# Kernel optimization log

Measured on AMD Instinct MI355X. Metric: run time of the kernel, lower is better.

The kernel has to match this reference:

```python
import jax, jax.numpy as jnp
import numpy as np

B, H, W, C = 512, 7, 7, 768


def _conv3(v, k, b):
    # 1-channel conv1d, kernel size 3, padding 1. v: (B, L), k: (3,), b: scalar
    vp = jnp.pad(v, ((0, 0), (1, 1)))
    return k[0] * vp[:, :-2] + k[1] * vp[:, 1:-1] + k[2] * vp[:, 2:] + b


def setup_inputs() -> dict:
    key = jax.random.key(0)
    ks = jax.random.split(key, 32)
    n = lambda i, shape, s=0.02: jax.random.normal(ks[i], shape, dtype=jnp.float32) * s
    inp = {
        "x": jax.random.normal(ks[0], (B, H, W, C), dtype=jnp.float32),
        # 1x1 Conv2d(dim,dim) weights stored as (out,in)
        "Wh": n(1, (C, C)), "bh": n(2, (C,)),
        "Ww": n(3, (C, C)), "bw": n(4, (C,)),
        "Ws": n(5, (C, C)), "bs": n(6, (C,)),
        # Conv1d(1,1,1) -> scalar weight/bias
        "convH_w": n(7, ()), "convH_b": n(8, ()),
        "convH2_k": n(9, (3,)), "convH2_b": n(10, ()),
        # Conv1d(2,1,1)
        "mixhw_k": n(11, (2,)), "mixhw_b": n(12, ()),
        "mixhw2_k": n(13, (3,)), "mixhw2_b": n(14, ()),
        # Conv1d(3,1,1)
        "mixhws_k": n(15, (3,)), "mixhws_b": n(16, ()),
        "mixhws2_k": n(17, (3,)), "mixhws2_b": n(18, ()),
        # Linear(7, dim)
        "linH_W": n(19, (C, 7), 0.1), "linH_b": n(20, (C,)),
        "linW_W": n(21, (C, 7), 0.1), "linW_b": n(22, (C,)),
        # mix_all: Conv2d(3*dim, dim, 1)
        "mixall_W": n(23, (C, 3 * C)), "mixall_b": n(24, (C,)),
        # proj: Linear(dim, dim)
        "proj_W": n(25, (C, C)), "proj_b": n(26, (C,)),
        "gate_weights": jnp.ones((2,), dtype=jnp.float32),
    }
    return inp


def reference(x, Wh, bh, Ww, bw, Ws, bs, convH_w, convH_b, convH2_k, convH2_b,
              mixhw_k, mixhw_b, mixhw2_k, mixhw2_b, mixhws_k, mixhws_b,
              mixhws2_k, mixhws2_b, linH_W, linH_b, linW_W, linW_b,
              mixall_W, mixall_b, proj_W, proj_b, gate_weights):
    gelu = lambda v: jax.nn.gelu(v, approximate=False)
    sig = jax.nn.sigmoid
    add = x

    # H branch: mlp_h (1x1 conv over channels), pool over (W, C) per H index
    h = gelu(jnp.einsum('bhwc,dc->bhwd', x, Wh) + bh)          # (B,H,W,C)
    h2v = h.mean(axis=(2, 3))                                   # (B,H)
    g_h = sig(_conv3(sig(h2v * convH_w + convH_b), convH2_k, convH2_b))  # (B,H)
    h3 = h * g_h[:, :, None, None]                              # gate per H index

    # W branch: pool over (H, C) per W index, gate mixed with H stats
    w = gelu(jnp.einsum('bhwc,dc->bhwd', x, Ww) + bw)           # (B,H,W,C)
    w2v = w.mean(axis=(1, 3))                                   # (B,W)
    g_hw = sig(_conv3(sig(mixhw_k[0] * h2v + mixhw_k[1] * w2v + mixhw_b),
                      mixhw2_k, mixhw2_b))                      # (B,W)
    w3 = w * g_hw[:, None, :, None]                             # gate per W index

    # C branch: pool over (H, W) per channel, gate mixed with lifted H/W stats
    s = gelu(jnp.einsum('bhwc,dc->bhwd', x, Ws) + bs)           # (B,H,W,C)
    s1v = s.mean(axis=(1, 2))                                   # (B,C)
    h2l = h2v @ linH_W.T + linH_b                               # (B,C)
    w2l = w2v @ linW_W.T + linW_b                               # (B,C)
    g_c = sig(_conv3(sig(mixhws_k[0] * h2l + mixhws_k[1] * w2l
                         + mixhws_k[2] * s1v + mixhws_b),
                     mixhws2_k, mixhws2_b))                     # (B,C)
    s2 = s * g_c[:, None, None, :]                              # gate per channel

    # concat along channel dim + 1x1 mixing conv + proj
    cat = jnp.concatenate([h3, w3, s2], axis=-1)                # (B,H,W,3C)
    mixed = jnp.einsum('bhwk,dk->bhwd', cat, mixall_W) + mixall_b
    out = mixed @ proj_W.T + proj_b
    out = out * gate_weights[0] + add * gate_weights[1]
    return out
```

## Files before the change

### kernel.cpp

```cpp
#include <hip/hip_runtime.h>
#include <cstdint>
#include <cstddef>

typedef __attribute__((ext_vector_type(8))) __bf16 bf16x8;
typedef __attribute__((ext_vector_type(4))) float f32x4;

__device__ __forceinline__ float sigm(float v) { return 1.0f / (1.0f + expf(-v)); }

__device__ __forceinline__ float gelu_fast(float v) {
  float u = v * (1.0f + 0.044715f * v * v);
  float z = 1.5957691216057308f * u;
  return v / (1.0f + __expf(-z));
}

__device__ __forceinline__ void async16(__bf16* lds, const __bf16* g) {
  __builtin_amdgcn_global_load_lds(
      (const __attribute__((address_space(1))) void*)g,
      (__attribute__((address_space(3))) void*)lds, 16, 0, 0);
}

__global__ __launch_bounds__(256) void k_convert(const float* __restrict__ src,
                                                 __bf16* __restrict__ dst, int n8) {
  int i = blockIdx.x * 256 + threadIdx.x;
  if (i >= n8) return;
  const f32x4* s4 = (const f32x4*)src;
  f32x4 a = s4[2 * i], b = s4[2 * i + 1];
  bf16x8 o;
#pragma unroll
  for (int e = 0; e < 4; ++e) { o[e] = (__bf16)a[e]; o[4 + e] = (__bf16)b[e]; }
  ((bf16x8*)dst)[i] = o;
}

__global__ __launch_bounds__(256) void k_bcat(const float* __restrict__ bh,
                                              const float* __restrict__ bw,
                                              const float* __restrict__ bs,
                                              float* __restrict__ bcat) {
  int i = blockIdx.x * 256 + threadIdx.x;
  if (i >= 2304) return;
  bcat[i] = i < 768 ? bh[i] : (i < 1536 ? bw[i - 768] : bs[i - 1536]);
}

__global__ __launch_bounds__(256) void k_transpose_cvt(const float* __restrict__ src,
                                                       __bf16* __restrict__ dst,
                                                       int R, int C) {
  __shared__ float t[32][33];
  const int c0 = blockIdx.x * 32, r0 = blockIdx.y * 32;
  const int tx = threadIdx.x, ty = threadIdx.y;
#pragma unroll
  for (int i = 0; i < 32; i += 8)
    if (r0 + ty + i < R && c0 + tx < C) t[ty + i][tx] = src[(size_t)(r0 + ty + i) * C + c0 + tx];
  __syncthreads();
#pragma unroll
  for (int i = 0; i < 32; i += 8)
    if (c0 + ty + i < C && r0 + tx < R)
      dst[(size_t)(c0 + ty + i) * R + r0 + tx] = (__bf16)t[tx][ty + i];
}

__global__ __launch_bounds__(256) void k_b2(const float* __restrict__ P,
                                            const float* __restrict__ bm,
                                            const float* __restrict__ pb,
                                            float* __restrict__ b2) {
  const int d = blockIdx.x * 256 + threadIdx.x;
  if (d >= 768) return;
  float acc = pb[d];
  const float* row = P + (size_t)d * 768;
#pragma unroll 4
  for (int c = 0; c < 768; c += 4) {
    f32x4 p4 = *(const f32x4*)(row + c);
    f32x4 b4 = *(const f32x4*)(bm + c);
    acc += p4[0] * b4[0] + p4[1] * b4[1] + p4[2] * b4[2] + p4[3] * b4[3];
  }
  b2[d] = acc;
}

template <int EPI>
__global__ __launch_bounds__(256, 2) void k_gemm(
    const __bf16* __restrict__ A, const __bf16* __restrict__ B,
    const float* __restrict__ bias, __bf16* __restrict__ outB,
    float* __restrict__ outF, const float* __restrict__ xres,
    const float* __restrict__ gatew, int N, int K) {
  __shared__ __bf16 lds[36864];
  const int tid = threadIdx.x;
  const int lane = tid & 63, wid = tid >> 6;
  const int wr = wid >> 1, wc = wid & 1;

  const int nwg = gridDim.x;
  const int q = nwg >> 3, r = nwg & 7;
  const int xcd = blockIdx.x & 7, bidx = blockIdx.x >> 3;
  const int wgid = (xcd < r ? xcd * (q + 1) : r * (q + 1) + (xcd - r) * q) + bidx;
  const int nTn = N >> 7;
  const int tm = wgid / nTn, tn = wgid % nTn;

  const __bf16* Ag = A + (size_t)tm * 256 * K;
  const __bf16* Bg = B + (size_t)tn * 128 * K;

  auto stage = [&](int buf, int kt) {
    const int base = buf * 12288;
#pragma unroll
    for (int j = 0; j < 4; ++j) {
      const int lin = j * 256 + tid;
      const int row = lin >> 2, ch = lin & 3;
      async16(&lds[base + lin * 8],
              Ag + (size_t)row * K + kt * 32 + ((ch ^ (row & 3)) << 3));
    }
#pragma unroll
    for (int j = 0; j < 2; ++j) {
      const int lin = j * 256 + tid;
      const int row = lin >> 2, ch = lin & 3;
      async16(&lds[base + 8192 + lin * 8],
              Bg + (size_t)row * K + kt * 32 + ((ch ^ (row & 3)) << 3));
    }
  };

  f32x4 acc[8][4];
#pragma unroll
  for (int m = 0; m < 8; ++m)
#pragma unroll
    for (int n = 0; n < 4; ++n) acc[m][n] = f32x4{0.f, 0.f, 0.f, 0.f};

  const int kc = lane >> 4;
  const int rA = wr * 128 + (lane & 15);
  const int rB = wc * 64 + (lane & 15);
  const int chA = kc ^ (rA & 3);
  const int chB = kc ^ (rB & 3);
  const int NT = K >> 5;

  stage(0, 0);
  stage(1, 1);
  asm volatile("s_waitcnt vmcnt(6)" ::: "memory");
  __builtin_amdgcn_s_barrier();

  for (int t = 0; t < NT; ++t) {
    const int cb = (t % 3) * 12288;
    if (t + 2 < NT) stage((t + 2) % 3, t + 2);
    bf16x8 af[8], bfv[4];
#pragma unroll
    for (int m = 0; m < 8; ++m)
      af[m] = *(const bf16x8*)&lds[cb + (rA + m * 16) * 32 + chA * 8];
#pragma unroll
    for (int n = 0; n < 4; ++n)
      bfv[n] = *(const bf16x8*)&lds[cb + 8192 + (rB + n * 16) * 32 + chB * 8];
    __builtin_amdgcn_s_setprio(1);
#pragma unroll
    for (int m = 0; m < 8; ++m)
#pragma unroll
      for (int n = 0; n < 4; ++n)
        acc[m][n] = __builtin_amdgcn_mfma_f32_16x16x32_bf16(af[m], bfv[n], acc[m][n], 0, 0, 0);
    __builtin_amdgcn_s_setprio(0);
    if (t + 2 < NT) { asm volatile("s_waitcnt vmcnt(6)" ::: "memory"); }
    else            { asm volatile("s_waitcnt vmcnt(0)" ::: "memory"); }
    __builtin_amdgcn_s_barrier();
  }

  const int orow = (lane >> 4) * 4;
  const int ocol = lane & 15;
  float g0 = 0.f, g1 = 0.f;
  if constexpr (EPI == 2) { g0 = gatew[0]; g1 = gatew[1]; }
#pragma unroll
  for (int m = 0; m < 8; ++m) {
#pragma unroll
    for (int n = 0; n < 4; ++n) {
#pragma unroll
      for (int rr = 0; rr < 4; ++rr) {
        const int rg = tm * 256 + wr * 128 + m * 16 + orow + rr;
        const int cg = tn * 128 + wc * 64 + n * 16 + ocol;
        if constexpr (EPI == 0) {
          float v = acc[m][n][rr] + bias[cg];
          outB[(size_t)rg * N + cg] = (__bf16)gelu_fast(v);
        } else if constexpr (EPI == 2) {
          float v = acc[m][n][rr] + bias[cg];
          outF[(size_t)rg * N + cg] = g0 * v + g1 * xres[(size_t)rg * N + cg];
        } else {
          outB[(size_t)rg * N + cg] = (__bf16)acc[m][n][rr];
        }
      }
    }
  }
}

__global__ __launch_bounds__(256) void k_pool(const __bf16* __restrict__ hws,
                                              float* __restrict__ h2v,
                                              float* __restrict__ w2v,
                                              float* __restrict__ s1v) {
  const int b = blockIdx.x, t = threadIdx.x;
  const int lane = t & 63, wave = t >> 6;
  const size_t base = (size_t)b * 49 * 2304;
  float hloc[7], wloc[7];
#pragma unroll
  for (int i = 0; i < 7; ++i) { hloc[i] = 0.f; wloc[i] = 0.f; }
  float sacc[8], sacc2[8];
#pragma unroll
  for (int e = 0; e < 8; ++e) { sacc[e] = 0.f; sacc2[e] = 0.f; }

  const bool isH = t < 96, isW = (t >= 96 && t < 192);
  const int off1 = isH ? t * 8 : (isW ? 768 + (t - 96) * 8 : 1536 + (t - 192) * 8);
  const int off2 = 1536 + (64 + t) * 8;

#pragma unroll
  for (int p = 0; p < 49; ++p) {
    const int hi = p / 7, wi = p % 7;
    const __bf16* row = hws + base + (size_t)p * 2304;
    bf16x8 v = *(const bf16x8*)(row + off1);
    float s8 = 0.f;
#pragma unroll
    for (int e = 0; e < 8; ++e) s8 += (float)v[e];
    if (isH) hloc[hi] += s8;
    else if (isW) wloc[wi] += s8;
    else {
#pragma unroll
      for (int e = 0; e < 8; ++e) sacc[e] += (float)v[e];
    }
    if (t < 32) {
      bf16x8 v2 = *(const bf16x8*)(row + off2);
#pragma unroll
      for (int e = 0; e < 8; ++e) sacc2[e] += (float)v2[e];
    }
  }

  if (t >= 192) {
#pragma unroll
    for (int e = 0; e < 8; ++e)
      s1v[b * 768 + (t - 192) * 8 + e] = sacc[e] * (1.f / 49.f);
  }
  if (t < 32) {
#pragma unroll
    for (int e = 0; e < 8; ++e)
      s1v[b * 768 + 512 + t * 8 + e] = sacc2[e] * (1.f / 49.f);
  }

  __shared__ float red[4][14];
#pragma unroll
  for (int i = 0; i < 7; ++i) {
    float hv = hloc[i], wv = wloc[i];
#pragma unroll
    for (int s = 32; s; s >>= 1) { hv += __shfl_xor(hv, s); wv += __shfl_xor(wv, s); }
    if (lane == 0) { red[wave][i] = hv; red[wave][7 + i] = wv; }
  }
  __syncthreads();
  if (t < 7) {
    h2v[b * 7 + t] = (red[0][t] + red[1][t] + red[2][t] + red[3][t]) * (1.f / 5376.f);
  } else if (t >= 16 && t < 23) {
    const int i = t - 16;
    w2v[b * 7 + i] =
        (red[0][7 + i] + red[1][7 + i] + red[2][7 + i] + red[3][7 + i]) * (1.f / 5376.f);
  }
}

__global__ __launch_bounds__(256) void k_gates(
    const float* __restrict__ h2v, const float* __restrict__ w2v,
    const float* __restrict__ s1v, const float* __restrict__ convH_w,
    const float* __restrict__ convH_b, const float* __restrict__ convH2_k,
    const float* __restrict__ convH2_b, const float* __restrict__ mixhw_k,
    const float* __restrict__ mixhw_b, const float* __restrict__ mixhw2_k,
    const float* __restrict__ mixhw2_b, const float* __restrict__ mixhws_k,
    const float* __restrict__ mixhws_b, const float* __restrict__ mixhws2_k,
    const float* __restrict__ mixhws2_b, const float* __restrict__ linHW,
    const float* __restrict__ linHb, const float* __restrict__ linWW,
    const float* __restrict__ linWb, float* __restrict__ g_h,
    float* __restrict__ g_hw, float* __restrict__ g_c) {
  const int b = blockIdx.x, t = threadIdx.x;
  __shared__ float hv[7], wv[7];
  __shared__ float tc[770];
  if (t < 7) { hv[t] = h2v[b * 7 + t]; wv[t] = w2v[b * 7 + t]; }
  if (t == 7) { tc[0] = 0.f; tc[769] = 0.f; }
  __syncthreads();

  if (t < 7) {
    const float cw = convH_w[0], cbv = convH_b[0];
    const float k0 = convH2_k[0], k1 = convH2_k[1], k2 = convH2_k[2], b2 = convH2_b[0];
    const float um = t > 0 ? sigm(hv[t - 1] * cw + cbv) : 0.f;
    const float u0 = sigm(hv[t] * cw + cbv);
    const float up = t < 6 ? sigm(hv[t + 1] * cw + cbv) : 0.f;
    g_h[b * 7 + t] = sigm(k0 * um + k1 * u0 + k2 * up + b2);

    const float a0 = mixhw_k[0], a1 = mixhw_k[1], ab = mixhw_b[0];
    const float q0 = mixhw2_k[0], q1 = mixhw2_k[1], q2 = mixhw2_k[2], qb = mixhw2_b[0];
    const float vm = t > 0 ? sigm(a0 * hv[t - 1] + a1 * wv[t - 1] + ab) : 0.f;
    const float v0 = sigm(a0 * hv[t] + a1 * wv[t] + ab);
    const float vp = t < 6 ? sigm(a0 * hv[t + 1] + a1 * wv[t + 1] + ab) : 0.f;
    g_hw[b * 7 + t] = sigm(q0 * vm + q1 * v0 + q2 * vp + qb);
  }

  const float m0 = mixhws_k[0], m1 = mixhws_k[1], m2 = mixhws_k[2], mb = mixhws_b[0];
#pragma unroll
  for (int j = 0; j < 3; ++j) {
    const int c = t + j * 256;
    float h2l = linHb[c], w2l = linWb[c];
#pragma unroll
    for (int i = 0; i < 7; ++i) {
      h2l += hv[i] * linHW[c * 7 + i];
      w2l += wv[i] * linWW[c * 7 + i];
    }
    tc[1 + c] = sigm(m0 * h2l + m1 * w2l + m2 * s1v[b * 768 + c] + mb);
  }
  __syncthreads();
  const float r0 = mixhws2_k[0], r1 = mixhws2_k[1], r2 = mixhws2_k[2], rb2 = mixhws2_b[0];
#pragma unroll
  for (int j = 0; j < 3; ++j) {
    const int c = t + j * 256;
    g_c[b * 768 + c] = sigm(r0 * tc[c] + r1 * tc[c + 1] + r2 * tc[c + 2] + rb2);
  }
}

__global__ __launch_bounds__(256) void k_gapply(__bf16* __restrict__ hws,
                                                const float* __restrict__ g_h,
                                                const float* __restrict__ g_hw,
                                                const float* __restrict__ g_c) {
  const int idx = blockIdx.x * 256 + threadIdx.x;
  const int k8 = idx % 288;
  const int p = idx / 288;
  const int b = p / 49, pp = p % 49;
  bf16x8* ptr = (bf16x8*)hws + idx;
  bf16x8 v = *ptr;
  if (k8 < 96) {
    const float g = g_h[b * 7 + pp / 7];
#pragma unroll
    for (int e = 0; e < 8; ++e) v[e] = (__bf16)((float)v[e] * g);
  } else if (k8 < 192) {
    const float g = g_hw[b * 7 + pp % 7];
#pragma unroll
    for (int e = 0; e < 8; ++e) v[e] = (__bf16)((float)v[e] * g);
  } else {
    const float* gcp = g_c + b * 768 + (k8 - 192) * 8;
#pragma unroll
    for (int e = 0; e < 8; ++e) v[e] = (__bf16)((float)v[e] * gcp[e]);
  }
  *ptr = v;
}

extern "C" void kernel_launch(void* const* d_in, const int* in_sizes, int n_in,
                              void* d_out, int out_size, void* d_ws, size_t ws_size,
                              hipStream_t stream) {
  const float* x        = (const float*)d_in[0];
  const float* Wh       = (const float*)d_in[1];
  const float* bh       = (const float*)d_in[2];
  const float* Ww       = (const float*)d_in[3];
  const float* bw       = (const float*)d_in[4];
  const float* Ws       = (const float*)d_in[5];
  const float* bs       = (const float*)d_in[6];
  const float* convH_w  = (const float*)d_in[7];
  const float* convH_b  = (const float*)d_in[8];
  const float* convH2_k = (const float*)d_in[9];
  const float* convH2_b = (const float*)d_in[10];
  const float* mixhw_k  = (const float*)d_in[11];
  const float* mixhw_b  = (const float*)d_in[12];
  const float* mixhw2_k = (const float*)d_in[13];
  const float* mixhw2_b = (const float*)d_in[14];
  const float* mixhws_k = (const float*)d_in[15];
  const float* mixhws_b = (const float*)d_in[16];
  const float* mixhws2_k= (const float*)d_in[17];
  const float* mixhws2_b= (const float*)d_in[18];
  const float* linHW    = (const float*)d_in[19];
  const float* linHb    = (const float*)d_in[20];
  const float* linWW    = (const float*)d_in[21];
  const float* linWb    = (const float*)d_in[22];
  const float* mixallW  = (const float*)d_in[23];
  const float* mixallb  = (const float*)d_in[24];
  const float* projW    = (const float*)d_in[25];
  const float* projb    = (const float*)d_in[26];
  const float* gatew    = (const float*)d_in[27];
  float* out = (float*)d_out;
  (void)in_sizes; (void)n_in; (void)out_size; (void)ws_size;

  const int M = 25088;
  char* ws = (char*)d_ws;
  size_t off = 0;
  auto carve = [&](size_t bytes) -> void* {
    void* p = ws + off;
    off += (bytes + 255) & ~(size_t)255;
    return p;
  };
  __bf16* xb     = (__bf16*)carve((size_t)M * 768 * 2);
  __bf16* Wcat   = (__bf16*)carve((size_t)2304 * 768 * 2);
  __bf16* Pb     = (__bf16*)carve((size_t)768 * 768 * 2);
  __bf16* Dt     = (__bf16*)carve((size_t)2304 * 768 * 2);
  __bf16* W2     = (__bf16*)carve((size_t)768 * 2304 * 2);
  float*  bcat   = (float*)carve(2304 * 4);
  float*  b2     = (float*)carve(768 * 4);
  __bf16* hws    = (__bf16*)carve((size_t)M * 2304 * 2);
  float*  h2v    = (float*)carve(512 * 7 * 4);
  float*  w2v    = (float*)carve(512 * 7 * 4);
  float*  s1v    = (float*)carve(512 * 768 * 4);
  float*  gh     = (float*)carve(512 * 7 * 4);
  float*  ghw    = (float*)carve(512 * 7 * 4);
  float*  gc     = (float*)carve(512 * 768 * 4);

  k_convert<<<9408, 256, 0, stream>>>(x, xb, (M * 768) / 8);
  k_convert<<<288, 256, 0, stream>>>(Wh, Wcat, 73728);
  k_convert<<<288, 256, 0, stream>>>(Ww, Wcat + 589824, 73728);
  k_convert<<<288, 256, 0, stream>>>(Ws, Wcat + 1179648, 73728);
  k_convert<<<288, 256, 0, stream>>>(projW, Pb, 73728);
  k_transpose_cvt<<<dim3(72, 24), dim3(32, 8), 0, stream>>>(mixallW, Dt, 768, 2304);
  k_bcat<<<9, 256, 0, stream>>>(bh, bw, bs, bcat);
  k_b2<<<3, 256, 0, stream>>>(projW, mixallb, projb, b2);

  k_gemm<3><<<3 * 18, 256, 0, stream>>>(Pb, Dt, nullptr, W2, nullptr, nullptr,
                                        nullptr, 2304, 768);
  k_gemm<0><<<98 * 18, 256, 0, stream>>>(xb, Wcat, bcat, hws, nullptr, nullptr,
                                         nullptr, 2304, 768);
  k_pool<<<512, 256, 0, stream>>>(hws, h2v, w2v, s1v);
  k_gates<<<512, 256, 0, stream>>>(h2v, w2v, s1v, convH_w, convH_b, convH2_k,
                                   convH2_b, mixhw_k, mixhw_b, mixhw2_k, mixhw2_b,
                                   mixhws_k, mixhws_b, mixhws2_k, mixhws2_b,
                                   linHW, linHb, linWW, linWb, gh, ghw, gc);
  k_gapply<<<28224, 256, 0, stream>>>(hws, gh, ghw, gc);
  k_gemm<2><<<98 * 6, 256, 0, stream>>>(hws, W2, b2, nullptr, out, x,
                                        gatew, 768, 2304);
}
```

Before: 415.1 us.

## Fold per-row H/W gates into final GEMM accumulator scaling, gate only S slice

Instead of rewriting all 2304 gated channels of hws, the H and W gates (which are per-row scalars) are applied by rescaling the GEMM accumulator at the K-segment boundaries (multiply by gh/ghw after the H segment, then by ghw after the W segment). Only the channel-gated S slice is materialized into a new buffer, and the final GEMM reads the S part from it. The LDS swizzle is also changed to use (row>>1)&3. Dividing gh by ghw risks precision loss or blowup if ghw is tiny.

```diff
diff --git a/kernel.cpp b/kernel.cpp
--- a/kernel.cpp
+++ b/kernel.cpp
@@ -78,7 +78,9 @@
     const __bf16* __restrict__ A, const __bf16* __restrict__ B,
     const float* __restrict__ bias, __bf16* __restrict__ outB,
     float* __restrict__ outF, const float* __restrict__ xres,
-    const float* __restrict__ gatew, int N, int K) {
+    const float* __restrict__ gatew, int N, int K,
+    const __bf16* __restrict__ A2, const float* __restrict__ ghr,
+    const float* __restrict__ ghwr) {
   __shared__ __bf16 lds[36864];
   const int tid = threadIdx.x;
   const int lane = tid & 63, wid = tid >> 6;
@@ -92,23 +94,31 @@
   const int tm = wgid / nTn, tn = wgid % nTn;
 
   const __bf16* Ag = A + (size_t)tm * 256 * K;
+  const __bf16* A2g = (EPI == 4) ? A2 + (size_t)tm * 256 * 768 : nullptr;
   const __bf16* Bg = B + (size_t)tn * 128 * K;
+
+  const int NT = K >> 5;
+  const int tb1 = NT / 3, tb2 = (2 * NT) / 3;
 
   auto stage = [&](int buf, int kt) {
     const int base = buf * 12288;
+    const bool useA2 = (EPI == 4) && (kt >= tb2);
 #pragma unroll
     for (int j = 0; j < 4; ++j) {
       const int lin = j * 256 + tid;
       const int row = lin >> 2, ch = lin & 3;
-      async16(&lds[base + lin * 8],
-              Ag + (size_t)row * K + kt * 32 + ((ch ^ (row & 3)) << 3));
+      const int sc = (ch ^ ((row >> 1) & 3)) << 3;
+      const __bf16* src = useA2
+          ? A2g + (size_t)row * 768 + (kt - tb2) * 32 + sc
+          : Ag + (size_t)row * K + kt * 32 + sc;
+      async16(&lds[base + lin * 8], src);
     }
 #pragma unroll
     for (int j = 0; j < 2; ++j) {
       const int lin = j * 256 + tid;
       const int row = lin >> 2, ch = lin & 3;
       async16(&lds[base + 8192 + lin * 8],
-              Bg + (size_t)row * K + kt * 32 + ((ch ^ (row & 3)) << 3));
+              Bg + (size_t)row * K + kt * 32 + ((ch ^ ((row >> 1) & 3)) << 3));
     }
   };
 
@@ -121,9 +131,9 @@
   const int kc = lane >> 4;
   const int rA = wr * 128 + (lane & 15);
   const int rB = wc * 64 + (lane & 15);
-  const int chA = kc ^ (rA & 3);
-  const int chB = kc ^ (rB & 3);
-  const int NT = K >> 5;
+  const int chA = kc ^ ((rA >> 1) & 3);
+  const int chB = kc ^ ((rB >> 1) & 3);
+  const int orow = (lane >> 4) * 4;
 
   stage(0, 0);
   stage(1, 1);
@@ -147,15 +157,37 @@
       for (int n = 0; n < 4; ++n)
         acc[m][n] = __builtin_amdgcn_mfma_f32_16x16x32_bf16(af[m], bfv[n], acc[m][n], 0, 0, 0);
     __builtin_amdgcn_s_setprio(0);
+    if constexpr (EPI == 4) {
+      if (t == tb1 - 1) {
+#pragma unroll
+        for (int m = 0; m < 8; ++m)
+#pragma unroll
+          for (int rr = 0; rr < 4; ++rr) {
+            const int rg = tm * 256 + wr * 128 + m * 16 + orow + rr;
+            const float f = ghr[rg] / ghwr[rg];
+#pragma unroll
+            for (int n = 0; n < 4; ++n) acc[m][n][rr] *= f;
+          }
+      } else if (t == tb2 - 1) {
+#pragma unroll
+        for (int m = 0; m < 8; ++m)
+#pragma unroll
+          for (int rr = 0; rr < 4; ++rr) {
+            const int rg = tm * 256 + wr * 128 + m * 16 + orow + rr;
+            const float f = ghwr[rg];
+#pragma unroll
+            for (int n = 0; n < 4; ++n) acc[m][n][rr] *= f;
+          }
+      }
+    }
     if (t + 2 < NT) { asm volatile("s_waitcnt vmcnt(6)" ::: "memory"); }
     else            { asm volatile("s_waitcnt vmcnt(0)" ::: "memory"); }
     __builtin_amdgcn_s_barrier();
   }
 
-  const int orow = (lane >> 4) * 4;
   const int ocol = lane & 15;
   float g0 = 0.f, g1 = 0.f;
-  if constexpr (EPI == 2) { g0 = gatew[0]; g1 = gatew[1]; }
+  if constexpr (EPI == 4) { g0 = gatew[0]; g1 = gatew[1]; }
 #pragma unroll
   for (int m = 0; m < 8; ++m) {
 #pragma unroll
@@ -167,7 +199,7 @@
         if constexpr (EPI == 0) {
           float v = acc[m][n][rr] + bias[cg];
           outB[(size_t)rg * N + cg] = (__bf16)gelu_fast(v);
-        } else if constexpr (EPI == 2) {
+        } else if constexpr (EPI == 4) {
           float v = acc[m][n][rr] + bias[cg];
           outF[(size_t)rg * N + cg] = g0 * v + g1 * xres[(size_t)rg * N + cg];
         } else {
@@ -256,10 +288,11 @@
     const float* __restrict__ mixhws_b, const float* __restrict__ mixhws2_k,
     const float* __restrict__ mixhws2_b, const float* __restrict__ linHW,
     const float* __restrict__ linHb, const float* __restrict__ linWW,
-    const float* __restrict__ linWb, float* __restrict__ g_h,
-    float* __restrict__ g_hw, float* __restrict__ g_c) {
+    const float* __restrict__ linWb, float* __restrict__ ghr,
+    float* __restrict__ ghwr, float* __restrict__ g_c) {
   const int b = blockIdx.x, t = threadIdx.x;
   __shared__ float hv[7], wv[7];
+  __shared__ float ghs[7], ghws[7];
   __shared__ float tc[770];
   if (t < 7) { hv[t] = h2v[b * 7 + t]; wv[t] = w2v[b * 7 + t]; }
   if (t == 7) { tc[0] = 0.f; tc[769] = 0.f; }
@@ -271,14 +304,14 @@
     const float um = t > 0 ? sigm(hv[t - 1] * cw + cbv) : 0.f;
     const float u0 = sigm(hv[t] * cw + cbv);
     const float up = t < 6 ? sigm(hv[t + 1] * cw + cbv) : 0.f;
-    g_h[b * 7 + t] = sigm(k0 * um + k1 * u0 + k2 * up + b2);
+    ghs[t] = sigm(k0 * um + k1 * u0 + k2 * up + b2);
 
     const float a0 = mixhw_k[0], a1 = mixhw_k[1], ab = mixhw_b[0];
     const float q0 = mixhw2_k[0], q1 = mixhw2_k[1], q2 = mixhw2_k[2], qb = mixhw2_b[0];
     const float vm = t > 0 ? sigm(a0 * hv[t - 1] + a1 * wv[t - 1] + ab) : 0.f;
     const float v0 = sigm(a0 * hv[t] + a1 * wv[t] + ab);
     const float vp = t < 6 ? sigm(a0 * hv[t + 1] + a1 * wv[t + 1] + ab) : 0.f;
-    g_hw[b * 7 + t] = sigm(q0 * vm + q1 * v0 + q2 * vp + qb);
+    ghws[t] = sigm(q0 * vm + q1 * v0 + q2 * vp + qb);
   }
 
   const float m0 = mixhws_k[0], m1 = mixhws_k[1], m2 = mixhws_k[2], mb = mixhws_b[0];
@@ -300,32 +333,30 @@
     const int c = t + j * 256;
     g_c[b * 768 + c] = sigm(r0 * tc[c] + r1 * tc[c + 1] + r2 * tc[c + 2] + rb2);
   }
-}
-
-__global__ __launch_bounds__(256) void k_gapply(__bf16* __restrict__ hws,
-                                                const float* __restrict__ g_h,
-                                                const float* __restrict__ g_hw,
-                                                const float* __restrict__ g_c) {
+  if (t < 49) {
+    ghr[b * 49 + t] = ghs[t / 7];
+    ghwr[b * 49 + t] = ghws[t % 7];
+  }
+}
+
+__global__ __launch_bounds__(256) void k_gapply_s(const __bf16* __restrict__ hws,
+                                                  const float* __restrict__ g_c,
+                                                  __bf16* __restrict__ sg) {
   const int idx = blockIdx.x * 256 + threadIdx.x;
-  const int k8 = idx % 288;
-  const int p = idx / 288;
-  const int b = p / 49, pp = p % 49;
-  bf16x8* ptr = (bf16x8*)hws + idx;
-  bf16x8 v = *ptr;
-  if (k8 < 96) {
-    const float g = g_h[b * 7 + pp / 7];
-#pragma unroll
-    for (int e = 0; e < 8; ++e) v[e] = (__bf16)((float)v[e] * g);
-  } else if (k8 < 192) {
-    const float g = g_hw[b * 7 + pp % 7];
-#pragma unroll
-    for (int e = 0; e < 8; ++e) v[e] = (__bf16)((float)v[e] * g);
-  } else {
-    const float* gcp = g_c + b * 768 + (k8 - 192) * 8;
-#pragma unroll
-    for (int e = 0; e < 8; ++e) v[e] = (__bf16)((float)v[e] * gcp[e]);
-  }
-  *ptr = v;
+  const int c8 = idx % 96;
+  const int r = idx / 96;
+  const int b = r / 49;
+  bf16x8 v = *(const bf16x8*)(hws + (size_t)r * 2304 + 1536 + c8 * 8);
+  const float* gcp = g_c + b * 768 + c8 * 8;
+  f32x4 gA = *(const f32x4*)gcp;
+  f32x4 gB = *(const f32x4*)(gcp + 4);
+  bf16x8 o;
+#pragma unroll
+  for (int e = 0; e < 4; ++e) {
+    o[e] = (__bf16)((float)v[e] * gA[e]);
+    o[4 + e] = (__bf16)((float)v[4 + e] * gB[e]);
+  }
+  ((bf16x8*)sg)[idx] = o;
 }
 
 extern "C" void kernel_launch(void* const* d_in, const int* in_sizes, int n_in,
@@ -378,11 +409,12 @@
   float*  bcat   = (float*)carve(2304 * 4);
   float*  b2     = (float*)carve(768 * 4);
   __bf16* hws    = (__bf16*)carve((size_t)M * 2304 * 2);
+  __bf16* sg     = (__bf16*)carve((size_t)M * 768 * 2);
   float*  h2v    = (float*)carve(512 * 7 * 4);
   float*  w2v    = (float*)carve(512 * 7 * 4);
   float*  s1v    = (float*)carve(512 * 768 * 4);
-  float*  gh     = (float*)carve(512 * 7 * 4);
-  float*  ghw    = (float*)carve(512 * 7 * 4);
+  float*  ghr    = (float*)carve((size_t)M * 4);
+  float*  ghwr   = (float*)carve((size_t)M * 4);
   float*  gc     = (float*)carve(512 * 768 * 4);
 
   k_convert<<<9408, 256, 0, stream>>>(x, xb, (M * 768) / 8);
@@ -395,15 +427,15 @@
   k_b2<<<3, 256, 0, stream>>>(projW, mixallb, projb, b2);
 
   k_gemm<3><<<3 * 18, 256, 0, stream>>>(Pb, Dt, nullptr, W2, nullptr, nullptr,
-                                        nullptr, 2304, 768);
+                                        nullptr, 2304, 768, nullptr, nullptr, nullptr);
   k_gemm<0><<<98 * 18, 256, 0, stream>>>(xb, Wcat, bcat, hws, nullptr, nullptr,
-                                         nullptr, 2304, 768);
+                                         nullptr, 2304, 768, nullptr, nullptr, nullptr);
   k_pool<<<512, 256, 0, stream>>>(hws, h2v, w2v, s1v);
   k_gates<<<512, 256, 0, stream>>>(h2v, w2v, s1v, convH_w, convH_b, convH2_k,
                                    convH2_b, mixhw_k, mixhw_b, mixhw2_k, mixhw2_b,
                                    mixhws_k, mixhws_b, mixhws2_k, mixhws2_b,
-                                   linHW, linHb, linWW, linWb, gh, ghw, gc);
-  k_gapply<<<28224, 256, 0, stream>>>(hws, gh, ghw, gc);
-  k_gemm<2><<<98 * 6, 256, 0, stream>>>(hws, W2, b2, nullptr, out, x,
-                                        gatew, 768, 2304);
-}
+                                   linHW, linHb, linWW, linWb, ghr, ghwr, gc);
+  k_gapply_s<<<9408, 256, 0, stream>>>(hws, gc, sg);
+  k_gemm<4><<<98 * 6, 256, 0, stream>>>(hws, W2, b2, nullptr, out, x,
+                                        gatew, 768, 2304, sg, ghr, ghwr);
+}
```

After: 1.008 ms. 143% more time.
